# Optimization experiments

Hardware: AMD Instinct MI355X
Metric: run time of the kernel (lower is better)

Reference implementation:

```python
import jax, jax.numpy as jnp
import numpy as np

B, T, IN, H, OUT = 128, 256, 1, 5000, 20


def setup_inputs() -> dict:
    key = jax.random.key(0)
    k1, k2, k3, k4, k5 = jax.random.split(key, 5)
    return {
        "x": jax.random.normal(k1, (B, T, IN), dtype=jnp.float32),
        "W_in": jax.random.normal(k2, (H, IN), dtype=jnp.float32) * (1.0 / np.sqrt(IN)),
        "b_in": jax.random.normal(k3, (H,), dtype=jnp.float32) * 0.01,
        "W_out": jax.random.normal(k4, (OUT, H), dtype=jnp.float32) * (1.0 / np.sqrt(H)),
        "b_out": jax.random.normal(k5, (OUT,), dtype=jnp.float32) * 0.01,
    }


def reference(x, W_in, b_in, W_out, b_out):
    # x: [B, T, IN]; recurrence: h_{t+1} = tanh(x_t @ W_in^T + b_in + h_t)
    batch = x.shape[0]
    hidden = W_in.shape[0]
    h0 = jnp.zeros((batch, hidden), dtype=x.dtype)
    xs = jnp.swapaxes(x, 0, 1)  # [T, B, IN] for scan over time

    def step(h, x_t):
        h_new = jnp.tanh(x_t @ W_in.T + b_in + h)
        return h_new, None

    h_final, _ = jax.lax.scan(step, h0, xs)
    logits = h_final @ W_out.T + b_out  # [B, OUT]
    return jax.nn.softmax(logits, axis=-1)
```

## Files before the change

### kernel.cpp

```cpp
#include <hip/hip_runtime.h>

#define T_STEPS 256
#define BATCH   128
#define HIDDEN  5000
#define NHALF   2500
#define NOUT    20
#define NBLK    10

__global__ __launch_bounds__(256)
void rnn_fused(const float* __restrict__ x,
               const float* __restrict__ W_in,
               const float* __restrict__ b_in,
               const float* __restrict__ W_out,
               float* __restrict__ part) {
    const int b   = blockIdx.y;
    const int tid = threadIdx.x;
    const int i0  = blockIdx.x * 256 + tid;
    const bool valid = (i0 < NHALF);
    const int j0 = valid ? i0 : 0;
    const int j1 = j0 + NHALF;

    const float c     = 2.8853900817779268f;
    const float inv_c = 0.34657359027997264f;
    const float n2c   = -5.7707801635558537f;

    const float wc0 = W_in[j0] * c;
    const float wc1 = W_in[j1] * c;
    const float K0  = __builtin_amdgcn_exp2f(b_in[j0] * c);
    const float K1  = __builtin_amdgcn_exp2f(b_in[j1] * c);

    const float* __restrict__ xrow = x + b * T_STEPS;

    float hc0 = 0.0f, hc1 = 0.0f;
    #pragma unroll 16
    for (int t = 0; t < T_STEPS; ++t) {
        const float xv = xrow[t];
        float u0 = fmaf(xv, wc0, hc0);
        float u1 = fmaf(xv, wc1, hc1);
        float e0 = __builtin_amdgcn_exp2f(u0);
        float e1 = __builtin_amdgcn_exp2f(u1);
        float d0 = fmaf(e0, K0, 1.0f);
        float d1 = fmaf(e1, K1, 1.0f);
        float r0 = __builtin_amdgcn_rcpf(d0);
        float r1 = __builtin_amdgcn_rcpf(d1);
        hc0 = fmaf(r0, n2c, c);
        hc1 = fmaf(r1, n2c, c);
    }
    const float h0 = valid ? hc0 * inv_c : 0.0f;
    const float h1 = valid ? hc1 * inv_c : 0.0f;

    float acc[NOUT];
    #pragma unroll
    for (int o = 0; o < NOUT; ++o) {
        const float w0 = W_out[o * HIDDEN + j0];
        const float w1 = W_out[o * HIDDEN + j1];
        acc[o] = fmaf(h0, w0, h1 * w1);
    }

    #pragma unroll
    for (int o = 0; o < NOUT; ++o) {
        #pragma unroll
        for (int s = 32; s > 0; s >>= 1)
            acc[o] += __shfl_down(acc[o], s, 64);
    }

    __shared__ float red[4][NOUT];
    const int wid = tid >> 6, lane = tid & 63;
    if (lane == 0) {
        #pragma unroll
        for (int o = 0; o < NOUT; ++o) red[wid][o] = acc[o];
    }
    __syncthreads();

    if (tid < NOUT) {
        const float v = red[0][tid] + red[1][tid] + red[2][tid] + red[3][tid];
        part[(b * NBLK + blockIdx.x) * NOUT + tid] = v;
    }
}

__global__ __launch_bounds__(64)
void softmax_head(const float* __restrict__ part,
                  const float* __restrict__ b_out,
                  float* __restrict__ out) {
    const int b = blockIdx.x;
    const int o = threadIdx.x;

    float v = -1e30f;
    if (o < NOUT) {
        float s = b_out[o];
        #pragma unroll
        for (int blk = 0; blk < NBLK; ++blk)
            s += part[(b * NBLK + blk) * NOUT + o];
        v = s;
    }

    float m = v;
    #pragma unroll
    for (int s = 32; s > 0; s >>= 1) m = fmaxf(m, __shfl_xor(m, s, 64));

    float e = (o < NOUT)
            ? __builtin_amdgcn_exp2f((v - m) * 1.4426950408889634f)
            : 0.0f;
    float ssum = e;
    #pragma unroll
    for (int s = 32; s > 0; s >>= 1) ssum += __shfl_xor(ssum, s, 64);

    if (o < NOUT) out[b * NOUT + o] = e / ssum;
}

extern "C" void kernel_launch(void* const* d_in, const int* in_sizes, int n_in,
                              void* d_out, int out_size, void* d_ws, size_t ws_size,
                              hipStream_t stream) {
    const float* x     = (const float*)d_in[0];
    const float* W_in  = (const float*)d_in[1];
    const float* b_in  = (const float*)d_in[2];
    const float* W_out = (const float*)d_in[3];
    const float* b_out = (const float*)d_in[4];
    float* out  = (float*)d_out;
    float* part = (float*)d_ws;

    dim3 grid1(NBLK, BATCH);
    rnn_fused<<<grid1, 256, 0, stream>>>(x, W_in, b_in, W_out, part);
    softmax_head<<<BATCH, 64, 0, stream>>>(part, b_out, out);
}
```

Measured before the change: 97.83 us.

## Replace transcendental exp2/rcp with packed-FMA polynomial exp and Newton reciprocal

```diff
diff --git a/kernel.cpp b/kernel.cpp
--- a/kernel.cpp
+++ b/kernel.cpp
@@ -6,6 +6,8 @@
 #define NHALF   2500
 #define NOUT    20
 #define NBLK    10
+
+typedef float v2f __attribute__((ext_vector_type(2)));
 
 __global__ __launch_bounds__(256)
 void rnn_fused(const float* __restrict__ x,
@@ -22,32 +24,60 @@
 
     const float c     = 2.8853900817779268f;
     const float inv_c = 0.34657359027997264f;
-    const float n2c   = -5.7707801635558537f;
 
-    const float wc0 = W_in[j0] * c;
-    const float wc1 = W_in[j1] * c;
-    const float K0  = __builtin_amdgcn_exp2f(b_in[j0] * c);
-    const float K1  = __builtin_amdgcn_exp2f(b_in[j1] * c);
+    const v2f C7 = {1.5252733804059840e-05f, 1.5252733804059840e-05f};
+    const v2f C6 = {1.5403530393381609e-04f, 1.5403530393381609e-04f};
+    const v2f C5 = {1.3333558146428443e-03f, 1.3333558146428443e-03f};
+    const v2f C4 = {9.6181291076284772e-03f, 9.6181291076284772e-03f};
+    const v2f C3 = {5.5504108664821580e-02f, 5.5504108664821580e-02f};
+    const v2f C2 = {2.4022650695910072e-01f, 2.4022650695910072e-01f};
+    const v2f C1 = {6.9314718055994531e-01f, 6.9314718055994531e-01f};
+    const v2f C0 = {1.0f, 1.0f};
+    const v2f BIG = {12582912.0f, 12582912.0f};
+    const v2f ONE = {1.0f, 1.0f};
+    const v2f TWO = {2.0f, 2.0f};
+    const v2f N2C = {-5.7707801635558537f, -5.7707801635558537f};
+
+    const v2f wc  = { W_in[j0] * c, W_in[j1] * c };
+    const v2f cb  = { b_in[j0] * c, b_in[j1] * c };
+    const v2f cpb = { c + cb.x, c + cb.y };
 
     const float* __restrict__ xrow = x + b * T_STEPS;
 
-    float hc0 = 0.0f, hc1 = 0.0f;
-    #pragma unroll 16
+    v2f s = cb;
+    #pragma unroll 8
     for (int t = 0; t < T_STEPS; ++t) {
         const float xv = xrow[t];
-        float u0 = fmaf(xv, wc0, hc0);
-        float u1 = fmaf(xv, wc1, hc1);
-        float e0 = __builtin_amdgcn_exp2f(u0);
-        float e1 = __builtin_amdgcn_exp2f(u1);
-        float d0 = fmaf(e0, K0, 1.0f);
-        float d1 = fmaf(e1, K1, 1.0f);
-        float r0 = __builtin_amdgcn_rcpf(d0);
-        float r1 = __builtin_amdgcn_rcpf(d1);
-        hc0 = fmaf(r0, n2c, c);
-        hc1 = fmaf(r1, n2c, c);
+        const v2f xv2 = {xv, xv};
+        v2f u  = __builtin_elementwise_fma(xv2, wc, s);
+        v2f k  = u + BIG;
+        v2f fl = k - BIG;
+        v2f tt = u - fl;
+        v2f p  = __builtin_elementwise_fma(tt, C7, C6);
+        p = __builtin_elementwise_fma(tt, p, C5);
+        p = __builtin_elementwise_fma(tt, p, C4);
+        p = __builtin_elementwise_fma(tt, p, C3);
+        p = __builtin_elementwise_fma(tt, p, C2);
+        p = __builtin_elementwise_fma(tt, p, C1);
+        p = __builtin_elementwise_fma(tt, p, C0);
+        v2f sc = { __uint_as_float((__float_as_uint(k.x) << 23) + 0x3F800000u),
+                   __uint_as_float((__float_as_uint(k.y) << 23) + 0x3F800000u) };
+        v2f E  = p * sc;
+        v2f d  = E + ONE;
+        v2f y  = { __uint_as_float(0x7EF311C3u - __float_as_uint(d.x)),
+                   __uint_as_float(0x7EF311C3u - __float_as_uint(d.y)) };
+        v2f e  = __builtin_elementwise_fma(-d, y, TWO);
+        y = y * e;
+        e = __builtin_elementwise_fma(-d, y, TWO);
+        y = y * e;
+        e = __builtin_elementwise_fma(-d, y, ONE);
+        y = __builtin_elementwise_fma(e, y, y);
+        s = __builtin_elementwise_fma(y, N2C, cpb);
     }
-    const float h0 = valid ? hc0 * inv_c : 0.0f;
-    const float h1 = valid ? hc1 * inv_c : 0.0f;
+
+    float h0 = (s.x - cb.x) * inv_c;
+    float h1 = (s.y - cb.y) * inv_c;
+    if (!valid) { h0 = 0.0f; h1 = 0.0f; }
 
     float acc[NOUT];
     #pragma unroll
@@ -60,8 +90,8 @@
     #pragma unroll
     for (int o = 0; o < NOUT; ++o) {
         #pragma unroll
-        for (int s = 32; s > 0; s >>= 1)
-            acc[o] += __shfl_down(acc[o], s, 64);
+        for (int sft = 32; sft > 0; sft >>= 1)
+            acc[o] += __shfl_down(acc[o], sft, 64);
     }
 
     __shared__ float red[4][NOUT];
@@ -96,14 +126,14 @@
 
     float m = v;
     #pragma unroll
-    for (int s = 32; s > 0; s >>= 1) m = fmaxf(m, __shfl_xor(m, s, 64));
+    for (int sft = 32; sft > 0; sft >>= 1) m = fmaxf(m, __shfl_xor(m, sft, 64));
 
     float e = (o < NOUT)
             ? __builtin_amdgcn_exp2f((v - m) * 1.4426950408889634f)
             : 0.0f;
     float ssum = e;
     #pragma unroll
-    for (int s = 32; s > 0; s >>= 1) ssum += __shfl_xor(ssum, s, 64);
+    for (int sft = 32; sft > 0; sft >>= 1) ssum += __shfl_xor(ssum, sft, 64);
 
     if (o < NOUT) out[b * NOUT + o] = e / ssum;
 }
```

New measurement: 126.1 us. 28.9% more time.

## Use one hidden unit per thread and replace rcp with Newton reciprocal

Applied to the files above, without the earlier changes.

```diff
diff --git a/kernel.cpp b/kernel.cpp
--- a/kernel.cpp
+++ b/kernel.cpp
@@ -3,9 +3,8 @@
 #define T_STEPS 256
 #define BATCH   128
 #define HIDDEN  5000
-#define NHALF   2500
 #define NOUT    20
-#define NBLK    10
+#define NBLK    20
 
 __global__ __launch_bounds__(256)
 void rnn_fused(const float* __restrict__ x,
@@ -16,52 +15,46 @@
     const int b   = blockIdx.y;
     const int tid = threadIdx.x;
     const int i0  = blockIdx.x * 256 + tid;
-    const bool valid = (i0 < NHALF);
+    const bool valid = (i0 < HIDDEN);
     const int j0 = valid ? i0 : 0;
-    const int j1 = j0 + NHALF;
 
     const float c     = 2.8853900817779268f;
     const float inv_c = 0.34657359027997264f;
-    const float n2c   = -5.7707801635558537f;
+    const float p2c   = 5.7707801635558537f;
 
-    const float wc0 = W_in[j0] * c;
-    const float wc1 = W_in[j1] * c;
-    const float K0  = __builtin_amdgcn_exp2f(b_in[j0] * c);
-    const float K1  = __builtin_amdgcn_exp2f(b_in[j1] * c);
+    const float wc  = W_in[j0] * c;
+    const float cb  = b_in[j0] * c;
+    const float cpb = c + cb;
 
     const float* __restrict__ xrow = x + b * T_STEPS;
 
-    float hc0 = 0.0f, hc1 = 0.0f;
-    #pragma unroll 16
+    float s = cb;
+
+    #pragma unroll 8
     for (int t = 0; t < T_STEPS; ++t) {
         const float xv = xrow[t];
-        float u0 = fmaf(xv, wc0, hc0);
-        float u1 = fmaf(xv, wc1, hc1);
-        float e0 = __builtin_amdgcn_exp2f(u0);
-        float e1 = __builtin_amdgcn_exp2f(u1);
-        float d0 = fmaf(e0, K0, 1.0f);
-        float d1 = fmaf(e1, K1, 1.0f);
-        float r0 = __builtin_amdgcn_rcpf(d0);
-        float r1 = __builtin_amdgcn_rcpf(d1);
-        hc0 = fmaf(r0, n2c, c);
-        hc1 = fmaf(r1, n2c, c);
+        const float u  = fmaf(xv, wc, s);
+        const float E  = __builtin_amdgcn_exp2f(u);
+        const float d  = E + 1.0f;
+        float y = __uint_as_float(0x7EF311C3u - __float_as_uint(d));
+        y = y * fmaf(d, y, -2.0f);
+        y = y * fmaf(d, y,  2.0f);
+        s = fmaf(y, p2c, cpb);
     }
-    const float h0 = valid ? hc0 * inv_c : 0.0f;
-    const float h1 = valid ? hc1 * inv_c : 0.0f;
+
+    float h = valid ? (s - cb) * inv_c : 0.0f;
 
     float acc[NOUT];
     #pragma unroll
     for (int o = 0; o < NOUT; ++o) {
-        const float w0 = W_out[o * HIDDEN + j0];
-        const float w1 = W_out[o * HIDDEN + j1];
-        acc[o] = fmaf(h0, w0, h1 * w1);
+        acc[o] = h * W_out[o * HIDDEN + j0];
     }
 
     #pragma unroll
     for (int o = 0; o < NOUT; ++o) {
         #pragma unroll
-        for (int s = 32; s > 0; s >>= 1)
-            acc[o] += __shfl_down(acc[o], s, 64);
+        for (int sft = 32; sft > 0; sft >>= 1)
+            acc[o] += __shfl_down(acc[o], sft, 64);
     }
 
     __shared__ float red[4][NOUT];
@@ -96,14 +89,14 @@
 
     float m = v;
     #pragma unroll
-    for (int s = 32; s > 0; s >>= 1) m = fmaxf(m, __shfl_xor(m, s, 64));
+    for (int sft = 32; sft > 0; sft >>= 1) m = fmaxf(m, __shfl_xor(m, sft, 64));
 
     float e = (o < NOUT)
             ? __builtin_amdgcn_exp2f((v - m) * 1.4426950408889634f)
             : 0.0f;
     float ssum = e;
     #pragma unroll
-    for (int s = 32; s > 0; s >>= 1) ssum += __shfl_xor(ssum, s, 64);
+    for (int sft = 32; sft > 0; sft >>= 1) ssum += __shfl_xor(ssum, sft, 64);
 
     if (o < NOUT) out[b * NOUT + o] = e / ssum;
 }
```

New measurement: 103.8 us. 6.1% more time.
